# Optimization experiments

Measured on AMD Instinct MI355X. Metric: run time of the kernel, lower is better.

## Reference

```python
import jax, jax.numpy as jnp
import numpy as np

N = 40000      # nodes
E = 640000     # edges (avg degree 16)
D = 128        # feature dim (in_features == all hidden_dims due to residual)


def setup_inputs() -> dict:
    key = jax.random.key(0)
    ks = jax.random.split(key, 8)
    xavier = (6.0 / (D + D)) ** 0.5
    return {
        "x": jax.random.normal(ks[0], (N, D), dtype=jnp.float32),
        "edge_index": jax.random.randint(ks[1], (2, E), 0, N, dtype=jnp.int64),
        "W_t": jax.random.uniform(ks[2], (D, D), jnp.float32, -xavier, xavier),
        "b_t": jnp.zeros((D,), jnp.float32),
        "W0": jax.random.uniform(ks[3], (D, D), jnp.float32, -xavier, xavier),
        "b0": jnp.zeros((D,), jnp.float32),
        "W1": jax.random.uniform(ks[4], (D, D), jnp.float32, -xavier, xavier),
        "b1": jnp.zeros((D,), jnp.float32),
    }


def _gcn_layer(h, row, col, W, b):
    # linear transform, then edge-wise gather + scatter-add aggregation
    z = jnp.matmul(h, W)                                  # [N, D]
    agg = jnp.zeros_like(z).at[row].add(z[col])           # out[row] += z[col]
    return jax.nn.relu(agg + b)


def reference(x, edge_index, W_t, b_t, W0, b0, W1, b1):
    row, col = edge_index[0], edge_index[1]
    h = jnp.matmul(x, W_t) + b_t                          # self.transform
    # residual GCN layers (dropout p=0.0 -> identity; eval mode)
    h = h + _gcn_layer(h, row, col, W0, b0)
    h = h + _gcn_layer(h, row, col, W1, b1)
    return h
```

## Files before the change

### kernel.cpp

```cpp
#include <hip/hip_runtime.h>
#include <hip/hip_bf16.h>

#define N_NODES 40000
#define N_EDGES 640000
#define DIM     128
#define NB      157
#define GEMMB   625
#define HEB     1250
#define NREP    4

typedef __attribute__((ext_vector_type(8))) short short8;
typedef __attribute__((ext_vector_type(4))) float f32x4;
typedef __attribute__((ext_vector_type(2))) float f32x2;

__device__ inline short f2bf(float f) {
    __hip_bfloat16 h = __float2bfloat16(f);
    return *reinterpret_cast<short*>(&h);
}
__device__ inline float bf2f(short u) {
    union { unsigned int i; float f; } x;
    x.i = ((unsigned int)(unsigned short)u) << 16;
    return x.f;
}

__device__ inline int fragidx(int k, int n) {
    int kb = k >> 5, kq = (k >> 3) & 3, j = k & 7;
    int nt = n >> 4, nl = n & 15;
    return (((kb * 8 + nt) * 64 + kq * 16 + nl) * 8 + j);
}

__global__ __launch_bounds__(256) void prep_zero(const float* __restrict__ Wt,
                                                 const float* __restrict__ W0,
                                                 const float* __restrict__ W1,
                                                 const float* __restrict__ bt,
                                                 short* __restrict__ WtF,
                                                 short* __restrict__ WfF,
                                                 short* __restrict__ W1F,
                                                 float* __restrict__ btf,
                                                 int* __restrict__ counts4,
                                                 int* __restrict__ flagtot) {
    int b = blockIdx.x;
    if (b < 64) {
        int gid = b * 256 + threadIdx.x;
        int k = gid >> 7, n = gid & 127;
        float wf = 0.f;
        for (int kk = 0; kk < 128; ++kk)
            wf += Wt[k * 128 + kk] * W0[kk * 128 + n];
        int fi = fragidx(k, n);
        WtF[fi] = f2bf(Wt[k * 128 + n]);
        W1F[fi] = f2bf(W1[k * 128 + n]);
        WfF[fi] = f2bf(wf);
        if (gid < 128) {
            float s = 0.f;
            for (int kk = 0; kk < 128; ++kk) s += bt[kk] * W0[kk * 128 + n];
            btf[n] = s;
        }
    } else if (b < 64 + NREP * NB) {
        int i = (b - 64) * 256 + threadIdx.x;
        if (i < NREP * N_NODES) counts4[i] = 0;
    } else {
        flagtot[threadIdx.x]       = 0;
        flagtot[threadIdx.x + 256] = 0;
    }
}

__global__ __launch_bounds__(256) void histrank_gemm(const int* __restrict__ rows,
                                                     int* __restrict__ counts4,
                                                     unsigned short* __restrict__ rank,
                                                     const float* __restrict__ A,
                                                     const short* __restrict__ WtF,
                                                     const short* __restrict__ WfF,
                                                     const float* __restrict__ bt,
                                                     const float* __restrict__ btf,
                                                     float* __restrict__ H,
                                                     __hip_bfloat16* __restrict__ Z) {
    if (blockIdx.x < HEB) {
        int gid = blockIdx.x * 256 + threadIdx.x;
        int* cnt = counts4 + (blockIdx.x & (NREP - 1)) * N_NODES;
#pragma unroll
        for (int h = 0; h < 2; ++h) {
            int e = gid + h * HEB * 256;
            int r = rows[e];
            rank[e] = (unsigned short)atomicAdd(&cnt[r], 1);
        }
        return;
    }

    const int t    = threadIdx.x;
    const int wave = t >> 6;
    const int l    = t & 63;
    const int nl   = l & 15;
    const int quad = l >> 4;
    const int wRow = (blockIdx.x - HEB) * 64 + wave * 16;

    f32x4 accH[8], accZ[8];
#pragma unroll
    for (int nt = 0; nt < 8; ++nt) {
        accH[nt] = (f32x4){0.f, 0.f, 0.f, 0.f};
        accZ[nt] = (f32x4){0.f, 0.f, 0.f, 0.f};
    }

#pragma unroll
    for (int kb = 0; kb < 4; ++kb) {
        const float* ap = A + (size_t)(wRow + nl) * 128 + kb * 32 + quad * 8;
        float4 f0 = *(const float4*)ap;
        float4 f1 = *(const float4*)(ap + 4);
        short8 afrag;
        afrag[0] = f2bf(f0.x); afrag[1] = f2bf(f0.y);
        afrag[2] = f2bf(f0.z); afrag[3] = f2bf(f0.w);
        afrag[4] = f2bf(f1.x); afrag[5] = f2bf(f1.y);
        afrag[6] = f2bf(f1.z); afrag[7] = f2bf(f1.w);
#pragma unroll
        for (int nt = 0; nt < 8; ++nt) {
            int off = ((kb * 8 + nt) * 64 + l) * 8;
            short8 bt_frag = *(const short8*)&WtF[off];
            short8 bf_frag = *(const short8*)&WfF[off];
            accH[nt] = __builtin_amdgcn_mfma_f32_16x16x32_bf16(afrag, bt_frag, accH[nt], 0, 0, 0);
            accZ[nt] = __builtin_amdgcn_mfma_f32_16x16x32_bf16(afrag, bf_frag, accZ[nt], 0, 0, 0);
        }
    }

#pragma unroll
    for (int nt = 0; nt < 8; ++nt) {
        int col = nt * 16 + nl;
        float bH = bt[col];
        float bZ = btf[col];
#pragma unroll
        for (int r = 0; r < 4; ++r) {
            int row = wRow + quad * 4 + r;
            H[(size_t)row * 128 + col] = accH[nt][r] + bH;
            *(short*)&Z[(size_t)row * 128 + col] = f2bf(accZ[nt][r] + bZ);
        }
    }
}

__global__ __launch_bounds__(256) void scan_onepass(const int* __restrict__ counts4,
                                                    int* __restrict__ flags,
                                                    int* __restrict__ totals,
                                                    int* __restrict__ row_ptr,
                                                    int* __restrict__ absOff) {
    __shared__ int sh[256];
    const int b = blockIdx.x;
    const int t = threadIdx.x;
    const int i = b * 256 + t;

    int c0 = 0, c1 = 0, c2 = 0, c3 = 0;
    if (i < N_NODES) {
        c0 = counts4[0 * N_NODES + i];
        c1 = counts4[1 * N_NODES + i];
        c2 = counts4[2 * N_NODES + i];
        c3 = counts4[3 * N_NODES + i];
    }
    const int c = c0 + c1 + c2 + c3;

    int val = c;
    sh[t] = val;
    __syncthreads();
    for (int off = 1; off < 256; off <<= 1) {
        int a = (t >= off) ? sh[t - off] : 0;
        __syncthreads();
        val += a;
        sh[t] = val;
        __syncthreads();
    }
    const int excl  = val - c;
    const int total = sh[255];

    if (t == 0) {
        atomicExch(&totals[b], total);
        __threadfence();
        atomicExch(&flags[b], 1);
    }

    int v = 0;
    if (t < NB) {
        while (atomicAdd(&flags[t], 0) == 0) { }
        v = atomicAdd(&totals[t], 0);
    }
    __syncthreads();
    int val2 = v;
    sh[t] = val2;
    __syncthreads();
    for (int off = 1; off < 256; off <<= 1) {
        int a = (t >= off) ? sh[t - off] : 0;
        __syncthreads();
        val2 += a;
        sh[t] = val2;
        __syncthreads();
    }
    int blkOff = (b == 0) ? 0 : sh[b - 1];

    if (i < N_NODES) {
        int base = excl + blkOff;
        row_ptr[i] = base;
        absOff[0 * N_NODES + i] = base;
        absOff[1 * N_NODES + i] = base + c0;
        absOff[2 * N_NODES + i] = base + c0 + c1;
        absOff[3 * N_NODES + i] = base + c0 + c1 + c2;
    }
    if (i == 0) row_ptr[N_NODES] = N_EDGES;
}

__global__ __launch_bounds__(256) void scatter_plain(const int* __restrict__ rows,
                                                     const int* __restrict__ cols,
                                                     const unsigned short* __restrict__ rank,
                                                     const int* __restrict__ absOff,
                                                     unsigned short* __restrict__ adj) {
    int gid = blockIdx.x * 256 + threadIdx.x;
    const int* off = absOff + (blockIdx.x & (NREP - 1)) * N_NODES;
#pragma unroll
    for (int h = 0; h < 2; ++h) {
        int e = gid + h * HEB * 256;
        int r = rows[e];
        adj[off[r] + (int)rank[e]] = (unsigned short)cols[e];
    }
}

__global__ __launch_bounds__(256) void agg0_gemm(const __hip_bfloat16* __restrict__ z0,
                                                 const int* __restrict__ row_ptr,
                                                 const unsigned short* __restrict__ adj,
                                                 const float* __restrict__ bias,
                                                 const short* __restrict__ W1F,
                                                 float* __restrict__ H,
                                                 unsigned char* __restrict__ Z1) {
    __shared__ short hs[16][136];

    const int t    = threadIdx.x;
    const int wave = t >> 6;
    const int l    = t & 63;
    const int quad = l >> 4;
    const int sl   = l & 15;
    const int nodeBase = blockIdx.x * 16;

#pragma unroll
    for (int u = 0; u < 4; ++u) {
        const int m    = wave * 4 + u;
        const int node = nodeBase + m;
        const int s = row_ptr[node];
        const int e = row_ptr[node + 1];

        float acc[8];
#pragma unroll
        for (int j = 0; j < 8; ++j) acc[j] = 0.f;

        int it = s + quad;
        for (; it + 12 < e; it += 16) {
            int c0 = adj[it];
            int c1 = adj[it + 4];
            int c2 = adj[it + 8];
            int c3 = adj[it + 12];
            short8 v0 = *(const short8*)&z0[(size_t)c0 * DIM + sl * 8];
            short8 v1 = *(const short8*)&z0[(size_t)c1 * DIM + sl * 8];
            short8 v2 = *(const short8*)&z0[(size_t)c2 * DIM + sl * 8];
            short8 v3 = *(const short8*)&z0[(size_t)c3 * DIM + sl * 8];
#pragma unroll
            for (int j = 0; j < 8; ++j)
                acc[j] += (bf2f(v0[j]) + bf2f(v1[j])) + (bf2f(v2[j]) + bf2f(v3[j]));
        }
        for (; it + 4 < e; it += 8) {
            int c0 = adj[it];
            int c1 = adj[it + 4];
            short8 v0 = *(const short8*)&z0[(size_t)c0 * DIM + sl * 8];
            short8 v1 = *(const short8*)&z0[(size_t)c1 * DIM + sl * 8];
#pragma unroll
            for (int j = 0; j < 8; ++j) acc[j] += bf2f(v0[j]) + bf2f(v1[j]);
        }
        if (it < e) {
            int c = adj[it];
            short8 v = *(const short8*)&z0[(size_t)c * DIM + sl * 8];
#pragma unroll
            for (int j = 0; j < 8; ++j) acc[j] += bf2f(v[j]);
        }

#pragma unroll
        for (int j = 0; j < 8; ++j) acc[j] += __shfl_xor(acc[j], 16, 64);
#pragma unroll
        for (int j = 0; j < 8; ++j) acc[j] += __shfl_xor(acc[j], 32, 64);

        if (quad == 0) {
            float* hp = H + (size_t)node * DIM + sl * 8;
            float4 h0 = *(float4*)hp;
            float4 h1 = *(float4*)(hp + 4);
            float4 b0v = *(const float4*)&bias[sl * 8];
            float4 b1v = *(const float4*)&bias[sl * 8 + 4];
            float r[8];
            r[0] = acc[0] + b0v.x; r[1] = acc[1] + b0v.y; r[2] = acc[2] + b0v.z; r[3] = acc[3] + b0v.w;
            r[4] = acc[4] + b1v.x; r[5] = acc[5] + b1v.y; r[6] = acc[6] + b1v.z; r[7] = acc[7] + b1v.w;
            float hn[8];
            hn[0] = h0.x; hn[1] = h0.y; hn[2] = h0.z; hn[3] = h0.w;
            hn[4] = h1.x; hn[5] = h1.y; hn[6] = h1.z; hn[7] = h1.w;
            short8 o;
#pragma unroll
            for (int j = 0; j < 8; ++j) {
                float rr = r[j] > 0.f ? r[j] : 0.f;
                hn[j] += rr;
                o[j] = f2bf(hn[j]);
            }
            *(float4*)hp       = make_float4(hn[0], hn[1], hn[2], hn[3]);
            *(float4*)(hp + 4) = make_float4(hn[4], hn[5], hn[6], hn[7]);
            *(short8*)&hs[m][sl * 8] = o;
        }
    }
    __syncthreads();

    f32x4 acc2[2];
    acc2[0] = (f32x4){0.f, 0.f, 0.f, 0.f};
    acc2[1] = (f32x4){0.f, 0.f, 0.f, 0.f};
#pragma unroll
    for (int kb = 0; kb < 4; ++kb) {
        short8 afrag = *(const short8*)&hs[sl][kb * 32 + quad * 8];
#pragma unroll
        for (int nt2 = 0; nt2 < 2; ++nt2) {
            int nt = wave * 2 + nt2;
            short8 bfrag = *(const short8*)&W1F[((kb * 8 + nt) * 64 + l) * 8];
            acc2[nt2] = __builtin_amdgcn_mfma_f32_16x16x32_bf16(afrag, bfrag, acc2[nt2], 0, 0, 0);
        }
    }
#pragma unroll
    for (int nt2 = 0; nt2 < 2; ++nt2) {
        int col = (wave * 2 + nt2) * 16 + sl;
#pragma unroll
        for (int r = 0; r < 4; ++r) {
            int row = nodeBase + quad * 4 + r;
            float v = acc2[nt2][r];
            int packed = __builtin_amdgcn_cvt_pk_fp8_f32(v, v, 0, false);
            Z1[(size_t)row * 128 + col] = (unsigned char)(packed & 0xFF);
        }
    }
}

__global__ __launch_bounds__(256) void agg_final(const unsigned char* __restrict__ z1,
                                                 const int* __restrict__ row_ptr,
                                                 const unsigned short* __restrict__ adj,
                                                 const float* __restrict__ bias,
                                                 float* __restrict__ H) {
    const int wave = threadIdx.x >> 6;
    const int l    = threadIdx.x & 63;
    const int quad = l >> 4;
    const int sl   = l & 15;
    const int node = blockIdx.x * 4 + wave;
    if (node >= N_NODES) return;

    const int s = row_ptr[node];
    const int e = row_ptr[node + 1];

    float acc[8];
#pragma unroll
    for (int j = 0; j < 8; ++j) acc[j] = 0.f;

#define ADD_FP8(u2)                                                          \
    {                                                                        \
        f32x2 a0 = __builtin_amdgcn_cvt_pk_f32_fp8((u2).x, false);           \
        f32x2 a1 = __builtin_amdgcn_cvt_pk_f32_fp8((u2).x, true);            \
        f32x2 a2 = __builtin_amdgcn_cvt_pk_f32_fp8((u2).y, false);           \
        f32x2 a3 = __builtin_amdgcn_cvt_pk_f32_fp8((u2).y, true);            \
        acc[0] += a0.x; acc[1] += a0.y; acc[2] += a1.x; acc[3] += a1.y;      \
        acc[4] += a2.x; acc[5] += a2.y; acc[6] += a3.x; acc[7] += a3.y;      \
    }

    int it = s + quad;
    for (; it + 12 < e; it += 16) {
        int c0 = adj[it];
        int c1 = adj[it + 4];
        int c2 = adj[it + 8];
        int c3 = adj[it + 12];
        uint2 v0 = *(const uint2*)&z1[(size_t)c0 * 128 + sl * 8];
        uint2 v1 = *(const uint2*)&z1[(size_t)c1 * 128 + sl * 8];
        uint2 v2 = *(const uint2*)&z1[(size_t)c2 * 128 + sl * 8];
        uint2 v3 = *(const uint2*)&z1[(size_t)c3 * 128 + sl * 8];
        ADD_FP8(v0); ADD_FP8(v1); ADD_FP8(v2); ADD_FP8(v3);
    }
    for (; it + 4 < e; it += 8) {
        int c0 = adj[it];
        int c1 = adj[it + 4];
        uint2 v0 = *(const uint2*)&z1[(size_t)c0 * 128 + sl * 8];
        uint2 v1 = *(const uint2*)&z1[(size_t)c1 * 128 + sl * 8];
        ADD_FP8(v0); ADD_FP8(v1);
    }
    if (it < e) {
        int c = adj[it];
        uint2 v = *(const uint2*)&z1[(size_t)c * 128 + sl * 8];
        ADD_FP8(v);
    }
#undef ADD_FP8

#pragma unroll
    for (int j = 0; j < 8; ++j) acc[j] += __shfl_xor(acc[j], 16, 64);
#pragma unroll
    for (int j = 0; j < 8; ++j) acc[j] += __shfl_xor(acc[j], 32, 64);

    if (quad == 0) {
        float* hp = H + (size_t)node * DIM + sl * 8;
        float4 h0 = *(float4*)hp;
        float4 h1 = *(float4*)(hp + 4);
        float4 b0 = *(const float4*)&bias[sl * 8];
        float4 b1 = *(const float4*)&bias[sl * 8 + 4];
        float r0 = acc[0] + b0.x, r1 = acc[1] + b0.y, r2 = acc[2] + b0.z, r3 = acc[3] + b0.w;
        float r4 = acc[4] + b1.x, r5 = acc[5] + b1.y, r6 = acc[6] + b1.z, r7 = acc[7] + b1.w;
        h0.x += r0 > 0.f ? r0 : 0.f;  h0.y += r1 > 0.f ? r1 : 0.f;
        h0.z += r2 > 0.f ? r2 : 0.f;  h0.w += r3 > 0.f ? r3 : 0.f;
        h1.x += r4 > 0.f ? r4 : 0.f;  h1.y += r5 > 0.f ? r5 : 0.f;
        h1.z += r6 > 0.f ? r6 : 0.f;  h1.w += r7 > 0.f ? r7 : 0.f;
        *(float4*)hp       = h0;
        *(float4*)(hp + 4) = h1;
    }
}

extern "C" void kernel_launch(void* const* d_in, const int* in_sizes, int n_in,
                              void* d_out, int out_size, void* d_ws, size_t ws_size,
                              hipStream_t stream) {
    const float* x   = (const float*)d_in[0];
    const int*   ei  = (const int*)d_in[1];
    const float* W_t = (const float*)d_in[2];
    const float* b_t = (const float*)d_in[3];
    const float* W0  = (const float*)d_in[4];
    const float* b0  = (const float*)d_in[5];
    const float* W1  = (const float*)d_in[6];
    const float* b1  = (const float*)d_in[7];

    const int* rows = ei;
    const int* cols = ei + N_EDGES;

    float* H = (float*)d_out;

    char* w = (char*)d_ws;
    __hip_bfloat16* Z0 = (__hip_bfloat16*)w;  w += (size_t)N_NODES * DIM * 2;
    unsigned char*  Z1 = (unsigned char*)w;   w += (size_t)N_NODES * DIM;
    short* WtF = (short*)w;  w += 128 * 128 * 2;
    short* WfF = (short*)w;  w += 128 * 128 * 2;
    short* W1F = (short*)w;  w += 128 * 128 * 2;
    float* btf = (float*)w;  w += 128 * 4;
    int* row_ptr = (int*)w;  w += (N_NODES + 1) * 4;
    int* counts4 = (int*)w;  w += NREP * N_NODES * 4;
    int* absOff  = (int*)w;  w += NREP * N_NODES * 4;
    int* flags   = (int*)w;  w += 256 * 4;
    int* totals  = (int*)w;  w += 256 * 4;
    unsigned short* rank = (unsigned short*)w;  w += (size_t)N_EDGES * 2;
    unsigned short* adj  = (unsigned short*)w;

    const int aggBlocks = (N_NODES + 3) / 4;

    prep_zero<<<64 + NREP * NB + 1, 256, 0, stream>>>(W_t, W0, W1, b_t, WtF, WfF,
                                                      W1F, btf, counts4, flags);

    histrank_gemm<<<HEB + GEMMB, 256, 0, stream>>>(rows, counts4, rank,
                                                   x, WtF, WfF, b_t, btf, H, Z0);

    scan_onepass<<<NB, 256, 0, stream>>>(counts4, flags, totals, row_ptr, absOff);

    scatter_plain<<<HEB, 256, 0, stream>>>(rows, cols, rank, absOff, adj);

    agg0_gemm<<<N_NODES / 16, 256, 0, stream>>>(Z0, row_ptr, adj, b0, W1F, H, Z1);

    agg_final<<<aggBlocks, 256, 0, stream>>>(Z1, row_ptr, adj, b1, H);
}
```

Before: 199.4 us.

## Replace global atomic histogram with per-chunk LDS byte-packed counters

```diff
diff --git a/kernel.cpp b/kernel.cpp
--- a/kernel.cpp
+++ b/kernel.cpp
@@ -7,7 +7,9 @@
 #define NB      157
 #define GEMMB   625
 #define HEB     1250
-#define NREP    4
+#define CHUNKS  64
+#define CHUNK_E 10000
+#define LDSW    10000
 
 typedef __attribute__((ext_vector_type(8))) short short8;
 typedef __attribute__((ext_vector_type(4))) float f32x4;
@@ -37,7 +39,6 @@
                                                  short* __restrict__ WfF,
                                                  short* __restrict__ W1F,
                                                  float* __restrict__ btf,
-                                                 int* __restrict__ counts4,
                                                  int* __restrict__ flagtot) {
     int b = blockIdx.x;
     if (b < 64) {
@@ -55,34 +56,42 @@
             for (int kk = 0; kk < 128; ++kk) s += bt[kk] * W0[kk * 128 + n];
             btf[n] = s;
         }
-    } else if (b < 64 + NREP * NB) {
-        int i = (b - 64) * 256 + threadIdx.x;
-        if (i < NREP * N_NODES) counts4[i] = 0;
     } else {
         flagtot[threadIdx.x]       = 0;
         flagtot[threadIdx.x + 256] = 0;
     }
 }
 
-__global__ __launch_bounds__(256) void histrank_gemm(const int* __restrict__ rows,
-                                                     int* __restrict__ counts4,
-                                                     unsigned short* __restrict__ rank,
-                                                     const float* __restrict__ A,
-                                                     const short* __restrict__ WtF,
-                                                     const short* __restrict__ WfF,
-                                                     const float* __restrict__ bt,
-                                                     const float* __restrict__ btf,
-                                                     float* __restrict__ H,
-                                                     __hip_bfloat16* __restrict__ Z) {
-    if (blockIdx.x < HEB) {
-        int gid = blockIdx.x * 256 + threadIdx.x;
-        int* cnt = counts4 + (blockIdx.x & (NREP - 1)) * N_NODES;
-#pragma unroll
-        for (int h = 0; h < 2; ++h) {
-            int e = gid + h * HEB * 256;
-            int r = rows[e];
-            rank[e] = (unsigned short)atomicAdd(&cnt[r], 1);
-        }
+__global__ __launch_bounds__(256) void histlds_gemm(const int* __restrict__ rows,
+                                                    unsigned char* __restrict__ rank8,
+                                                    unsigned int* __restrict__ cnt8w,
+                                                    const float* __restrict__ A,
+                                                    const short* __restrict__ WtF,
+                                                    const short* __restrict__ WfF,
+                                                    const float* __restrict__ bt,
+                                                    const float* __restrict__ btf,
+                                                    float* __restrict__ H,
+                                                    __hip_bfloat16* __restrict__ Z) {
+    __shared__ unsigned int lcnt[LDSW];
+
+    if (blockIdx.x < CHUNKS) {
+        for (int i = threadIdx.x; i < LDSW; i += 256) lcnt[i] = 0u;
+        __syncthreads();
+        const int base = blockIdx.x * CHUNK_E;
+#pragma unroll
+        for (int i = 0; i < 40; ++i) {
+            int o = i * 256 + threadIdx.x;
+            if (o < CHUNK_E) {
+                int e = base + o;
+                int r = rows[e];
+                unsigned int sh = (unsigned int)(r & 3) * 8u;
+                unsigned int old = atomicAdd(&lcnt[r >> 2], 1u << sh);
+                rank8[e] = (unsigned char)((old >> sh) & 0xFFu);
+            }
+        }
+        __syncthreads();
+        unsigned int* out = cnt8w + blockIdx.x * LDSW;
+        for (int i = threadIdx.x; i < LDSW; i += 256) out[i] = lcnt[i];
         return;
     }
 
@@ -91,7 +100,7 @@
     const int l    = t & 63;
     const int nl   = l & 15;
     const int quad = l >> 4;
-    const int wRow = (blockIdx.x - HEB) * 64 + wave * 16;
+    const int wRow = (blockIdx.x - CHUNKS) * 64 + wave * 16;
 
     f32x4 accH[8], accZ[8];
 #pragma unroll
@@ -134,26 +143,22 @@
     }
 }
 
-__global__ __launch_bounds__(256) void scan_onepass(const int* __restrict__ counts4,
+__global__ __launch_bounds__(256) void scan_onepass(unsigned char* __restrict__ cnt8,
                                                     int* __restrict__ flags,
                                                     int* __restrict__ totals,
-                                                    int* __restrict__ row_ptr,
-                                                    int* __restrict__ absOff) {
+                                                    int* __restrict__ row_ptr) {
     __shared__ int sh[256];
     const int b = blockIdx.x;
     const int t = threadIdx.x;
     const int i = b * 256 + t;
 
-    int c0 = 0, c1 = 0, c2 = 0, c3 = 0;
+    int deg = 0;
     if (i < N_NODES) {
-        c0 = counts4[0 * N_NODES + i];
-        c1 = counts4[1 * N_NODES + i];
-        c2 = counts4[2 * N_NODES + i];
-        c3 = counts4[3 * N_NODES + i];
-    }
-    const int c = c0 + c1 + c2 + c3;
-
-    int val = c;
+#pragma unroll 8
+        for (int c = 0; c < CHUNKS; ++c) deg += cnt8[(size_t)c * N_NODES + i];
+    }
+
+    int val = deg;
     sh[t] = val;
     __syncthreads();
     for (int off = 1; off < 256; off <<= 1) {
@@ -163,7 +168,7 @@
         sh[t] = val;
         __syncthreads();
     }
-    const int excl  = val - c;
+    const int excl  = val - deg;
     const int total = sh[255];
 
     if (t == 0) {
@@ -193,26 +198,31 @@
     if (i < N_NODES) {
         int base = excl + blkOff;
         row_ptr[i] = base;
-        absOff[0 * N_NODES + i] = base;
-        absOff[1 * N_NODES + i] = base + c0;
-        absOff[2 * N_NODES + i] = base + c0 + c1;
-        absOff[3 * N_NODES + i] = base + c0 + c1 + c2;
+        int run = 0;
+#pragma unroll 8
+        for (int c = 0; c < CHUNKS; ++c) {
+            int cv = cnt8[(size_t)c * N_NODES + i];
+            cnt8[(size_t)c * N_NODES + i] = (unsigned char)run;
+            run += cv;
+        }
     }
     if (i == 0) row_ptr[N_NODES] = N_EDGES;
 }
 
 __global__ __launch_bounds__(256) void scatter_plain(const int* __restrict__ rows,
                                                      const int* __restrict__ cols,
-                                                     const unsigned short* __restrict__ rank,
-                                                     const int* __restrict__ absOff,
+                                                     const unsigned char* __restrict__ rank8,
+                                                     const unsigned char* __restrict__ pref8,
+                                                     const int* __restrict__ row_ptr,
                                                      unsigned short* __restrict__ adj) {
     int gid = blockIdx.x * 256 + threadIdx.x;
-    const int* off = absOff + (blockIdx.x & (NREP - 1)) * N_NODES;
 #pragma unroll
     for (int h = 0; h < 2; ++h) {
         int e = gid + h * HEB * 256;
         int r = rows[e];
-        adj[off[r] + (int)rank[e]] = (unsigned short)cols[e];
+        int c = e / CHUNK_E;
+        int pos = row_ptr[r] + (int)pref8[(size_t)c * N_NODES + r] + (int)rank8[e];
+        adj[pos] = (unsigned short)cols[e];
     }
 }
 
@@ -431,24 +441,23 @@
     short* W1F = (short*)w;  w += 128 * 128 * 2;
     float* btf = (float*)w;  w += 128 * 4;
     int* row_ptr = (int*)w;  w += (N_NODES + 1) * 4;
-    int* counts4 = (int*)w;  w += NREP * N_NODES * 4;
-    int* absOff  = (int*)w;  w += NREP * N_NODES * 4;
     int* flags   = (int*)w;  w += 256 * 4;
     int* totals  = (int*)w;  w += 256 * 4;
-    unsigned short* rank = (unsigned short*)w;  w += (size_t)N_EDGES * 2;
+    unsigned int* cnt8w = (unsigned int*)w;  w += (size_t)CHUNKS * LDSW * 4;
+    unsigned char* rank8 = (unsigned char*)w;  w += (size_t)N_EDGES;
     unsigned short* adj  = (unsigned short*)w;
 
     const int aggBlocks = (N_NODES + 3) / 4;
 
-    prep_zero<<<64 + NREP * NB + 1, 256, 0, stream>>>(W_t, W0, W1, b_t, WtF, WfF,
-                                                      W1F, btf, counts4, flags);
-
-    histrank_gemm<<<HEB + GEMMB, 256, 0, stream>>>(rows, counts4, rank,
-                                                   x, WtF, WfF, b_t, btf, H, Z0);
-
-    scan_onepass<<<NB, 256, 0, stream>>>(counts4, flags, totals, row_ptr, absOff);
-
-    scatter_plain<<<HEB, 256, 0, stream>>>(rows, cols, rank, absOff, adj);
+    prep_zero<<<65, 256, 0, stream>>>(W_t, W0, W1, b_t, WtF, WfF, W1F, btf, flags);
+
+    histlds_gemm<<<CHUNKS + GEMMB, 256, 0, stream>>>(rows, rank8, cnt8w,
+                                                     x, WtF, WfF, b_t, btf, H, Z0);
+
+    scan_onepass<<<NB, 256, 0, stream>>>((unsigned char*)cnt8w, flags, totals, row_ptr);
+
+    scatter_plain<<<HEB, 256, 0, stream>>>(rows, cols, rank8, (unsigned char*)cnt8w,
+                                           row_ptr, adj);
 
     agg0_gemm<<<N_NODES / 16, 256, 0, stream>>>(Z0, row_ptr, adj, b0, W1F, H, Z1);
 
```

Measured after the change: 185.2 us. 7.1% less time.
